# Kernel optimization log

Hardware: AMD Instinct MI355X
Metric: run time of the kernel (lower is better)

Reference implementation:

```python
import jax, jax.numpy as jnp
import numpy as np

B, N, DIM, H = 2, 192, 512, 8
Dh = DIM // H
SCALE = Dh ** -0.5


def setup_inputs() -> dict:
    key = jax.random.key(0)
    ks = jax.random.split(key, 13)
    s = 0.02

    def w(k):
        return jax.random.normal(k, (DIM, DIM), dtype=jnp.float32) * s

    def b(k):
        return jax.random.normal(k, (DIM,), dtype=jnp.float32) * s

    return {
        "queries": jax.random.normal(ks[0], (B, N, DIM), dtype=jnp.float32),
        "keys": jax.random.normal(ks[1], (B, N, DIM), dtype=jnp.float32),
        "values": jax.random.normal(ks[2], (B, N, DIM), dtype=jnp.float32),
        "Wq": w(ks[3]), "bq": b(ks[4]),
        "Wk": w(ks[5]), "bk": b(ks[6]),
        "Wl": w(ks[7]), "bl": b(ks[8]),
        "Wv": w(ks[9]), "bv": b(ks[10]),
        "Wp": w(ks[11]), "bp": b(ks[12]),
    }


def _split_heads(x):
    # [B, N, DIM] -> [B, H, N, Dh]
    return x.reshape(B, N, H, Dh).transpose(0, 2, 1, 3)


def reference(queries, keys, values, Wq, bq, Wk, bk, Wl, bl, Wv, bv, Wp, bp):
    q = _split_heads(queries @ Wq.T + bq) * SCALE
    k = _split_heads(keys @ Wk.T + bk)
    l = _split_heads(keys @ Wl.T + bl)
    v = _split_heads(values @ Wv.T + bv)
    # third-order scores: [B, H, N, N, N]
    attn = jnp.einsum('bhid,bhjd,bhkd->bhijk', q, k, l)
    # softmax over flattened (j, k) axis (valid_lens=None path)
    attn = jax.nn.softmax(attn.reshape(B, H, N, N * N), axis=-1).reshape(B, H, N, N, N)
    # contraction with v_map[b,h,j,k,d] = v[b,h,j,d]*v[b,h,k,d], fused (same math)
    x = jnp.einsum('bhijk,bhjd,bhkd->bhid', attn, v, v)
    x = x.transpose(0, 2, 1, 3).reshape(B, N, DIM)  # merge heads
    return x @ Wp.T + bp
```

## Files before the change

### kernel.cpp

```cpp
#include <hip/hip_runtime.h>

#define B_ 2
#define N_ 192
#define DIM_ 512
#define H_ 8
#define DH_ 64
#define PROJ_ELEMS (B_*H_*N_*DH_)

typedef __bf16 bf16_t;
typedef __bf16 bf16x8 __attribute__((ext_vector_type(8)));
typedef float  f32x16 __attribute__((ext_vector_type(16)));

__device__ __forceinline__ f32x16 mfma32(bf16x8 a, bf16x8 b, f32x16 c) {
    return __builtin_amdgcn_mfma_f32_32x32x16_bf16(a, b, c, 0, 0, 0);
}

union U4 { unsigned int u[4]; bf16x8 v; };

__device__ __forceinline__ unsigned int pack_bf16(float a, float b) {
    unsigned short ua = __builtin_bit_cast(unsigned short, (bf16_t)a);
    unsigned short ub = __builtin_bit_cast(unsigned short, (bf16_t)b);
    return (unsigned int)ua | ((unsigned int)ub << 16);
}
__device__ __forceinline__ float bfbits(unsigned short u) {
    return (float)__builtin_bit_cast(bf16_t, u);
}

struct PArgs {
    const float* A[4];
    const float* W[4];
    const float* bias[4];
    float scale[4];
};

__global__ __launch_bounds__(256) void proj4_kernel(PArgs args, bf16_t* out) {
    const int wid = threadIdx.x >> 6, lane = threadIdx.x & 63;
    const int lo = lane & 31, hi = lane >> 5;
    const int gt  = blockIdx.x * 4 + wid;
    const int mat = gt / 192, t = gt % 192;
    const int r0 = (t >> 4) * 32, c0 = (t & 15) * 32;
    const int c = c0 + lo;

    const float* __restrict__ arow = args.A[mat] + (size_t)(r0 + lo) * DIM_;
    const float* __restrict__ wrow = args.W[mat] + (size_t)c * DIM_;

    f32x16 acc = {};
    for (int k0 = 0; k0 < DIM_; k0 += 16) {
        const int kk = k0 + hi * 8;
        float4 a0 = *(const float4*)(arow + kk);
        float4 a1 = *(const float4*)(arow + kk + 4);
        float4 b0 = *(const float4*)(wrow + kk);
        float4 b1 = *(const float4*)(wrow + kk + 4);
        bf16x8 af, bf;
        af[0]=(bf16_t)a0.x; af[1]=(bf16_t)a0.y; af[2]=(bf16_t)a0.z; af[3]=(bf16_t)a0.w;
        af[4]=(bf16_t)a1.x; af[5]=(bf16_t)a1.y; af[6]=(bf16_t)a1.z; af[7]=(bf16_t)a1.w;
        bf[0]=(bf16_t)b0.x; bf[1]=(bf16_t)b0.y; bf[2]=(bf16_t)b0.z; bf[3]=(bf16_t)b0.w;
        bf[4]=(bf16_t)b1.x; bf[5]=(bf16_t)b1.y; bf[6]=(bf16_t)b1.z; bf[7]=(bf16_t)b1.w;
        acc = mfma32(af, bf, acc);
    }
    const float bv = args.bias[mat][c];
    const float sc = args.scale[mat];
    const int h = c >> 6, d = c & 63;
    #pragma unroll
    for (int r = 0; r < 16; ++r) {
        int row = r0 + (r & 3) + 8 * (r >> 2) + 4 * hi;
        int bb = (row >= N_) ? 1 : 0;
        int n = row - bb * N_;
        out[(size_t)mat * PROJ_ELEMS + (((size_t)(bb * H_ + h)) * N_ + n) * DH_ + d] =
            (bf16_t)((acc[r] + bv) * sc);
    }
}

__global__ __launch_bounds__(256) void outproj_kernel(const bf16_t* __restrict__ X,
                                                      const float* __restrict__ Wp,
                                                      const float* __restrict__ bp,
                                                      float* __restrict__ out) {
    const int wid = threadIdx.x >> 6, lane = threadIdx.x & 63;
    const int lo = lane & 31, hi = lane >> 5;
    const int gt = blockIdx.x * 4 + wid;
    const int r0 = (gt >> 4) * 32, c0 = (gt & 15) * 32;
    const int c = c0 + lo;

    const bf16_t* __restrict__ xrow = X + (size_t)(r0 + lo) * DIM_;
    const float*  __restrict__ wrow = Wp + (size_t)c * DIM_;

    f32x16 acc = {};
    for (int k0 = 0; k0 < DIM_; k0 += 16) {
        const int kk = k0 + hi * 8;
        bf16x8 af = *(const bf16x8*)(xrow + kk);
        float4 b0 = *(const float4*)(wrow + kk);
        float4 b1 = *(const float4*)(wrow + kk + 4);
        bf16x8 bf;
        bf[0]=(bf16_t)b0.x; bf[1]=(bf16_t)b0.y; bf[2]=(bf16_t)b0.z; bf[3]=(bf16_t)b0.w;
        bf[4]=(bf16_t)b1.x; bf[5]=(bf16_t)b1.y; bf[6]=(bf16_t)b1.z; bf[7]=(bf16_t)b1.w;
        acc = mfma32(af, bf, acc);
    }
    const float bv = bp[c];
    #pragma unroll
    for (int r = 0; r < 16; ++r) {
        int row = r0 + (r & 3) + 8 * (r >> 2) + 4 * hi;
        out[(size_t)row * DIM_ + c] = acc[r] + bv;
    }
}

__global__ __launch_bounds__(256, 3) void attn_kernel(
    const bf16_t* __restrict__ Qg, const bf16_t* __restrict__ Kg,
    const bf16_t* __restrict__ Lg, const bf16_t* __restrict__ Vg,
    bf16_t* __restrict__ Xout)
{
    __shared__ __attribute__((aligned(16))) bf16_t Llds[192 * 72];
    __shared__ __attribute__((aligned(16))) bf16_t VTlds[64 * 200];

    const int bh = blockIdx.y;
    const int tid = threadIdx.x, wid = tid >> 6, lane = tid & 63;
    const int lo = lane & 31, hi = lane >> 5;
    const size_t base = (size_t)bh * (N_ * DH_);

    for (int idx = tid; idx < 1536; idx += 256) {
        int row = idx >> 3, ch = idx & 7;
        *(uint4*)&Llds[row * 72 + ch * 8] = *(const uint4*)(Lg + base + row * 64 + ch * 8);
    }
    for (int idx = tid; idx < 1536; idx += 256) {
        int dc = idx / 192, j = idx - dc * 192;
        bf16x8 v = *(const bf16x8*)(Vg + base + (size_t)j * 64 + dc * 8);
        #pragma unroll
        for (int u = 0; u < 8; ++u)
            VTlds[(dc * 8 + u) * 200 + j] = v[u];
    }
    __syncthreads();

    const int i = blockIdx.x * 4 + wid;
    const bf16_t* qp = Qg + base + (size_t)i * 64;
    bf16x8 qb[4];
    #pragma unroll
    for (int s = 0; s < 4; ++s) qb[s] = *(const bf16x8*)(qp + s * 16 + hi * 8);

    float xacc0 = 0.f, xacc1 = 0.f;
    float Zp[4] = {0.f, 0.f, 0.f, 0.f};

    for (int jb = 0; jb < 6; ++jb) {
        bf16x8 bq[4];
        const bf16_t* kp = Kg + base + (size_t)(jb * 32 + lo) * 64;
        #pragma unroll
        for (int s = 0; s < 4; ++s) {
            bf16x8 kv = *(const bf16x8*)(kp + s * 16 + hi * 8);
            bf16x8 t;
            #pragma unroll
            for (int u = 0; u < 8; ++u) t[u] = (bf16_t)((float)kv[u] * (float)qb[s][u]);
            bq[s] = t;
        }

        f32x16 Tc0 = {}, Tc1 = {};
        #pragma unroll
        for (int kh = 0; kh < 2; ++kh) {
            f32x16 Sc[3];
            #pragma unroll
            for (int kt = 0; kt < 3; ++kt) {
                f32x16 a = {};
                #pragma unroll
                for (int s = 0; s < 4; ++s) {
                    bf16x8 lf = *(const bf16x8*)&Llds[(kh * 96 + kt * 32 + lo) * 72 + s * 16 + hi * 8];
                    a = mfma32(lf, bq[s], a);
                }
                Sc[kt] = a;
            }
            #pragma unroll
            for (int kt = 0; kt < 3; ++kt) {
                float e[16];
                #pragma unroll
                for (int r = 0; r < 16; ++r) {
                    e[r] = __builtin_amdgcn_exp2f(Sc[kt][r]);
                    Zp[r & 3] += e[r];
                }
                #pragma unroll
                for (int sg = 0; sg < 2; ++sg) {
                    unsigned int x0 = pack_bf16(e[8*sg+0], e[8*sg+1]);
                    unsigned int x1 = pack_bf16(e[8*sg+2], e[8*sg+3]);
                    unsigned int y0 = pack_bf16(e[8*sg+4], e[8*sg+5]);
                    unsigned int y1 = pack_bf16(e[8*sg+6], e[8*sg+7]);
                    asm volatile("v_permlane32_swap_b32 %0, %1\n\t"
                                 "v_permlane32_swap_b32 %2, %3"
                                 : "+v"(x0), "+v"(y0), "+v"(x1), "+v"(y1));
                    U4 uf; uf.u[0] = x0; uf.u[1] = x1; uf.u[2] = y0; uf.u[3] = y1;
                    const int tg = kh * 6 + kt * 2 + sg;
                    bf16x8 vf0 = *(const bf16x8*)&VTlds[(0 * 32 + lo) * 200 + tg * 16 + hi * 8];
                    Tc0 = mfma32(uf.v, vf0, Tc0);
                    bf16x8 vf1 = *(const bf16x8*)&VTlds[(1 * 32 + lo) * 200 + tg * 16 + hi * 8];
                    Tc1 = mfma32(uf.v, vf1, Tc1);
                }
            }
        }
        #pragma unroll
        for (int m = 0; m < 4; ++m) {
            const int jj = jb * 32 + m * 8 + 4 * hi;
            ushort4 v0 = *(const ushort4*)&VTlds[(0 * 32 + lo) * 200 + jj];
            ushort4 v1 = *(const ushort4*)&VTlds[(1 * 32 + lo) * 200 + jj];
            xacc0 += Tc0[m*4+0]*bfbits(v0.x) + Tc0[m*4+1]*bfbits(v0.y)
                   + Tc0[m*4+2]*bfbits(v0.z) + Tc0[m*4+3]*bfbits(v0.w);
            xacc1 += Tc1[m*4+0]*bfbits(v1.x) + Tc1[m*4+1]*bfbits(v1.y)
                   + Tc1[m*4+2]*bfbits(v1.z) + Tc1[m*4+3]*bfbits(v1.w);
        }
    }

    float Z = (Zp[0] + Zp[1]) + (Zp[2] + Zp[3]);
    Z += __shfl_xor(Z, 1);
    Z += __shfl_xor(Z, 2);
    Z += __shfl_xor(Z, 4);
    Z += __shfl_xor(Z, 8);
    Z += __shfl_xor(Z, 16);
    Z += __shfl_xor(Z, 32);
    xacc0 += __shfl_xor(xacc0, 32);
    xacc1 += __shfl_xor(xacc1, 32);
    const float invZ = 1.0f / Z;

    if (hi == 0) {
        const int b = bh >> 3, h = bh & 7;
        bf16_t* op = Xout + ((size_t)(b * N_ + i) * DIM_) + h * 64;
        op[lo]      = (bf16_t)(xacc0 * invZ);
        op[32 + lo] = (bf16_t)(xacc1 * invZ);
    }
}

extern "C" void kernel_launch(void* const* d_in, const int* in_sizes, int n_in,
                              void* d_out, int out_size, void* d_ws, size_t ws_size,
                              hipStream_t stream) {
    (void)in_sizes; (void)n_in; (void)out_size; (void)ws_size;
    const float* queries = (const float*)d_in[0];
    const float* keys    = (const float*)d_in[1];
    const float* values  = (const float*)d_in[2];
    const float* Wq = (const float*)d_in[3];
    const float* bq = (const float*)d_in[4];
    const float* Wk = (const float*)d_in[5];
    const float* bk = (const float*)d_in[6];
    const float* Wl = (const float*)d_in[7];
    const float* bl = (const float*)d_in[8];
    const float* Wv = (const float*)d_in[9];
    const float* bv = (const float*)d_in[10];
    const float* Wp = (const float*)d_in[11];
    const float* bp = (const float*)d_in[12];

    bf16_t* Qw = (bf16_t*)d_ws;
    bf16_t* Xw = Qw + 4 * (size_t)PROJ_ELEMS;

    PArgs pa;
    pa.A[0] = queries; pa.W[0] = Wq; pa.bias[0] = bq; pa.scale[0] = 0.125f * 1.44269504f;
    pa.A[1] = keys;    pa.W[1] = Wk; pa.bias[1] = bk; pa.scale[1] = 1.0f;
    pa.A[2] = keys;    pa.W[2] = Wl; pa.bias[2] = bl; pa.scale[2] = 1.0f;
    pa.A[3] = values;  pa.W[3] = Wv; pa.bias[3] = bv; pa.scale[3] = 1.0f;
    proj4_kernel<<<dim3(192), 256, 0, stream>>>(pa, Qw);

    attn_kernel<<<dim3(48, 16), 256, 0, stream>>>(
        Qw, Qw + PROJ_ELEMS, Qw + 2 * (size_t)PROJ_ELEMS, Qw + 3 * (size_t)PROJ_ELEMS, Xw);

    outproj_kernel<<<dim3(48), 256, 0, stream>>>(Xw, Wp, bp, (float*)d_out);
}
```

Measured before the change: 151.5 us.

## Pre-convert inputs to bf16 and use LDS-tiled 64x64 GEMMs for projections

New measurement: 137.1 us. 1.1x faster.

```diff
diff --git a/kernel.cpp b/kernel.cpp
--- a/kernel.cpp
+++ b/kernel.cpp
@@ -6,8 +6,11 @@
 #define H_ 8
 #define DH_ 64
 #define PROJ_ELEMS (B_*H_*N_*DH_)
+#define W_ELEMS (DIM_*DIM_)
+#define A_ELEMS (B_*N_*DIM_)
 
 typedef __bf16 bf16_t;
+typedef __bf16 bf16x4 __attribute__((ext_vector_type(4)));
 typedef __bf16 bf16x8 __attribute__((ext_vector_type(8)));
 typedef float  f32x16 __attribute__((ext_vector_type(16)));
 
@@ -26,80 +29,95 @@
     return (float)__builtin_bit_cast(bf16_t, u);
 }
 
-struct PArgs {
-    const float* A[4];
-    const float* W[4];
+struct CArgs {
+    const float* src[8];
+    bf16_t* dst[8];
+    int n[8];
+};
+__global__ __launch_bounds__(256) void cvt_kernel(CArgs a) {
+    const int s = blockIdx.y;
+    const int i = (blockIdx.x * 256 + threadIdx.x) * 4;
+    if (i < a.n[s]) {
+        float4 v = *(const float4*)(a.src[s] + i);
+        bf16x4 o;
+        o[0] = (bf16_t)v.x; o[1] = (bf16_t)v.y; o[2] = (bf16_t)v.z; o[3] = (bf16_t)v.w;
+        *(bf16x4*)(a.dst[s] + i) = o;
+    }
+}
+
+struct GArgs {
+    const bf16_t* A[4];
+    const bf16_t* Bm[4];
     const float* bias[4];
     float scale[4];
 };
 
-__global__ __launch_bounds__(256) void proj4_kernel(PArgs args, bf16_t* out) {
-    const int wid = threadIdx.x >> 6, lane = threadIdx.x & 63;
+template<int MODE>
+__global__ __launch_bounds__(256) void gemm64_kernel(GArgs g, void* outp) {
+    const int mat = blockIdx.y;
+    const bf16_t* __restrict__ A  = g.A[mat];
+    const bf16_t* __restrict__ Bm = g.Bm[mat];
+
+    const int rt = blockIdx.x >> 3, ct = blockIdx.x & 7;
+    const int r0 = rt * 64, c0 = ct * 64;
+    const int tid = threadIdx.x, wid = tid >> 6, lane = tid & 63;
     const int lo = lane & 31, hi = lane >> 5;
-    const int gt  = blockIdx.x * 4 + wid;
-    const int mat = gt / 192, t = gt % 192;
-    const int r0 = (t >> 4) * 32, c0 = (t & 15) * 32;
-    const int c = c0 + lo;
-
-    const float* __restrict__ arow = args.A[mat] + (size_t)(r0 + lo) * DIM_;
-    const float* __restrict__ wrow = args.W[mat] + (size_t)c * DIM_;
+    const int wr = wid >> 1, wc = wid & 1;
+
+    __shared__ __attribute__((aligned(16))) bf16_t As[64 * 64];
+    __shared__ __attribute__((aligned(16))) bf16_t Bs[64 * 64];
 
     f32x16 acc = {};
-    for (int k0 = 0; k0 < DIM_; k0 += 16) {
-        const int kk = k0 + hi * 8;
-        float4 a0 = *(const float4*)(arow + kk);
-        float4 a1 = *(const float4*)(arow + kk + 4);
-        float4 b0 = *(const float4*)(wrow + kk);
-        float4 b1 = *(const float4*)(wrow + kk + 4);
-        bf16x8 af, bf;
-        af[0]=(bf16_t)a0.x; af[1]=(bf16_t)a0.y; af[2]=(bf16_t)a0.z; af[3]=(bf16_t)a0.w;
-        af[4]=(bf16_t)a1.x; af[5]=(bf16_t)a1.y; af[6]=(bf16_t)a1.z; af[7]=(bf16_t)a1.w;
-        bf[0]=(bf16_t)b0.x; bf[1]=(bf16_t)b0.y; bf[2]=(bf16_t)b0.z; bf[3]=(bf16_t)b0.w;
-        bf[4]=(bf16_t)b1.x; bf[5]=(bf16_t)b1.y; bf[6]=(bf16_t)b1.z; bf[7]=(bf16_t)b1.w;
-        acc = mfma32(af, bf, acc);
-    }
-    const float bv = args.bias[mat][c];
-    const float sc = args.scale[mat];
-    const int h = c >> 6, d = c & 63;
-    #pragma unroll
-    for (int r = 0; r < 16; ++r) {
-        int row = r0 + (r & 3) + 8 * (r >> 2) + 4 * hi;
-        int bb = (row >= N_) ? 1 : 0;
-        int n = row - bb * N_;
-        out[(size_t)mat * PROJ_ELEMS + (((size_t)(bb * H_ + h)) * N_ + n) * DH_ + d] =
-            (bf16_t)((acc[r] + bv) * sc);
-    }
-}
-
-__global__ __launch_bounds__(256) void outproj_kernel(const bf16_t* __restrict__ X,
-                                                      const float* __restrict__ Wp,
-                                                      const float* __restrict__ bp,
-                                                      float* __restrict__ out) {
-    const int wid = threadIdx.x >> 6, lane = threadIdx.x & 63;
-    const int lo = lane & 31, hi = lane >> 5;
-    const int gt = blockIdx.x * 4 + wid;
-    const int r0 = (gt >> 4) * 32, c0 = (gt & 15) * 32;
-    const int c = c0 + lo;
-
-    const bf16_t* __restrict__ xrow = X + (size_t)(r0 + lo) * DIM_;
-    const float*  __restrict__ wrow = Wp + (size_t)c * DIM_;
-
-    f32x16 acc = {};
-    for (int k0 = 0; k0 < DIM_; k0 += 16) {
-        const int kk = k0 + hi * 8;
-        bf16x8 af = *(const bf16x8*)(xrow + kk);
-        float4 b0 = *(const float4*)(wrow + kk);
-        float4 b1 = *(const float4*)(wrow + kk + 4);
-        bf16x8 bf;
-        bf[0]=(bf16_t)b0.x; bf[1]=(bf16_t)b0.y; bf[2]=(bf16_t)b0.z; bf[3]=(bf16_t)b0.w;
-        bf[4]=(bf16_t)b1.x; bf[5]=(bf16_t)b1.y; bf[6]=(bf16_t)b1.z; bf[7]=(bf16_t)b1.w;
-        acc = mfma32(af, bf, acc);
-    }
-    const float bv = bp[c];
-    #pragma unroll
-    for (int r = 0; r < 16; ++r) {
-        int row = r0 + (r & 3) + 8 * (r >> 2) + 4 * hi;
-        out[(size_t)row * DIM_ + c] = acc[r] + bv;
+    for (int k0 = 0; k0 < DIM_; k0 += 64) {
+        #pragma unroll
+        for (int cch = 0; cch < 2; ++cch) {
+            const int d = wid * 2048 + cch * 1024 + lane * 16;
+            const int r = d >> 7;
+            const int off = (d ^ ((r & 7) << 4)) & 127;
+            const char* srcA = (const char*)A + (size_t)(r0 + r) * (DIM_ * 2) + k0 * 2 + off;
+            const char* srcB = (const char*)Bm + (size_t)(c0 + r) * (DIM_ * 2) + k0 * 2 + off;
+            __builtin_amdgcn_global_load_lds(
+                (const __attribute__((address_space(1))) void*)srcA,
+                (__attribute__((address_space(3))) void*)((char*)As + wid * 2048 + cch * 1024),
+                16, 0, 0);
+            __builtin_amdgcn_global_load_lds(
+                (const __attribute__((address_space(1))) void*)srcB,
+                (__attribute__((address_space(3))) void*)((char*)Bs + wid * 2048 + cch * 1024),
+                16, 0, 0);
+        }
+        __syncthreads();
+        const int rowA = wr * 32 + lo, rowB = wc * 32 + lo;
+        #pragma unroll
+        for (int s = 0; s < 4; ++s) {
+            const int ka = (rowA * 128 + s * 32 + hi * 16) ^ ((rowA & 7) << 4);
+            const int kb = (rowB * 128 + s * 32 + hi * 16) ^ ((rowB & 7) << 4);
+            bf16x8 af = *(const bf16x8*)((const char*)As + ka);
+            bf16x8 bf = *(const bf16x8*)((const char*)Bs + kb);
+            acc = mfma32(af, bf, acc);
+        }
+        __syncthreads();
+    }
+
+    const int c = c0 + wc * 32 + lo;
+    const float bv = g.bias[mat][c];
+    if (MODE == 0) {
+        const float sc = g.scale[mat];
+        const int h = c >> 6, dd = c & 63;
+        bf16_t* out = (bf16_t*)outp + (size_t)mat * PROJ_ELEMS;
+        #pragma unroll
+        for (int r = 0; r < 16; ++r) {
+            int row = r0 + wr * 32 + (r & 3) + 8 * (r >> 2) + 4 * hi;
+            int bb = (row >= N_) ? 1 : 0;
+            int n = row - bb * N_;
+            out[(((size_t)(bb * H_ + h)) * N_ + n) * DH_ + dd] = (bf16_t)((acc[r] + bv) * sc);
+        }
+    } else {
+        float* out = (float*)outp;
+        #pragma unroll
+        for (int r = 0; r < 16; ++r) {
+            int row = r0 + wr * 32 + (r & 3) + 8 * (r >> 2) + 4 * hi;
+            out[(size_t)row * DIM_ + c] = acc[r] + bv;
+        }
     }
 }
 
@@ -239,18 +257,36 @@
     const float* Wp = (const float*)d_in[11];
     const float* bp = (const float*)d_in[12];
 
-    bf16_t* Qw = (bf16_t*)d_ws;
-    bf16_t* Xw = Qw + 4 * (size_t)PROJ_ELEMS;
-
-    PArgs pa;
-    pa.A[0] = queries; pa.W[0] = Wq; pa.bias[0] = bq; pa.scale[0] = 0.125f * 1.44269504f;
-    pa.A[1] = keys;    pa.W[1] = Wk; pa.bias[1] = bk; pa.scale[1] = 1.0f;
-    pa.A[2] = keys;    pa.W[2] = Wl; pa.bias[2] = bl; pa.scale[2] = 1.0f;
-    pa.A[3] = values;  pa.W[3] = Wv; pa.bias[3] = bv; pa.scale[3] = 1.0f;
-    proj4_kernel<<<dim3(192), 256, 0, stream>>>(pa, Qw);
+    bf16_t* Abf = (bf16_t*)d_ws;
+    bf16_t* Wbf = Abf + 3 * (size_t)A_ELEMS;
+    bf16_t* Pw  = Wbf + 5 * (size_t)W_ELEMS;
+    bf16_t* Xw  = Pw  + 4 * (size_t)PROJ_ELEMS;
+
+    CArgs ca;
+    ca.src[0] = queries; ca.dst[0] = Abf;               ca.n[0] = A_ELEMS;
+    ca.src[1] = keys;    ca.dst[1] = Abf + A_ELEMS;     ca.n[1] = A_ELEMS;
+    ca.src[2] = values;  ca.dst[2] = Abf + 2*A_ELEMS;   ca.n[2] = A_ELEMS;
+    ca.src[3] = Wq;      ca.dst[3] = Wbf;               ca.n[3] = W_ELEMS;
+    ca.src[4] = Wk;      ca.dst[4] = Wbf + W_ELEMS;     ca.n[4] = W_ELEMS;
+    ca.src[5] = Wl;      ca.dst[5] = Wbf + 2*W_ELEMS;   ca.n[5] = W_ELEMS;
+    ca.src[6] = Wv;      ca.dst[6] = Wbf + 3*W_ELEMS;   ca.n[6] = W_ELEMS;
+    ca.src[7] = Wp;      ca.dst[7] = Wbf + 4*W_ELEMS;   ca.n[7] = W_ELEMS;
+    cvt_kernel<<<dim3(256, 8), 256, 0, stream>>>(ca);
+
+    GArgs pa;
+    pa.A[0] = Abf;             pa.Bm[0] = Wbf;             pa.bias[0] = bq; pa.scale[0] = 0.125f * 1.44269504f;
+    pa.A[1] = Abf + A_ELEMS;   pa.Bm[1] = Wbf + W_ELEMS;   pa.bias[1] = bk; pa.scale[1] = 1.0f;
+    pa.A[2] = Abf + A_ELEMS;   pa.Bm[2] = Wbf + 2*W_ELEMS; pa.bias[2] = bl; pa.scale[2] = 1.0f;
+    pa.A[3] = Abf + 2*A_ELEMS; pa.Bm[3] = Wbf + 3*W_ELEMS; pa.bias[3] = bv; pa.scale[3] = 1.0f;
+    gemm64_kernel<0><<<dim3(48, 4), 256, 0, stream>>>(pa, (void*)Pw);
 
     attn_kernel<<<dim3(48, 16), 256, 0, stream>>>(
-        Qw, Qw + PROJ_ELEMS, Qw + 2 * (size_t)PROJ_ELEMS, Qw + 3 * (size_t)PROJ_ELEMS, Xw);
-
-    outproj_kernel<<<dim3(48), 256, 0, stream>>>(Xw, Wp, bp, (float*)d_out);
-}
+        Pw, Pw + PROJ_ELEMS, Pw + 2 * (size_t)PROJ_ELEMS, Pw + 3 * (size_t)PROJ_ELEMS, Xw);
+
+    GArgs fa;
+    fa.A[0] = Xw; fa.Bm[0] = Wbf + 4*W_ELEMS; fa.bias[0] = bp; fa.scale[0] = 1.0f;
+    fa.A[1] = fa.A[0]; fa.Bm[1] = fa.Bm[0]; fa.bias[1] = fa.bias[0]; fa.scale[1] = 1.0f;
+    fa.A[2] = fa.A[0]; fa.Bm[2] = fa.Bm[0]; fa.bias[2] = fa.bias[0]; fa.scale[2] = 1.0f;
+    fa.A[3] = fa.A[0]; fa.Bm[3] = fa.Bm[0]; fa.bias[3] = fa.bias[0]; fa.scale[3] = 1.0f;
+    gemm64_kernel<1><<<dim3(48, 1), 256, 0, stream>>>(fa, d_out);
+}
```
